# Optimization experiments

Measured on AMD Instinct MI355X. Metric: run time of the kernel, lower is better.

The kernel has to match this reference:

```python
import jax, jax.numpy as jnp
import numpy as np
from jax import lax

THRESH = 1.0
MIN_VMEM = -1.0

def _conv(x, w, stride):
    # x: [N,C,H,W], w: [O,I,kh,kw]
    return lax.conv_general_dilated(
        x, w, window_strides=(stride, stride), padding=((1, 1), (1, 1)),
        dimension_numbers=("NCHW", "OIHW", "NCHW"))

def _avgpool2(x):
    n, c, h, w = x.shape
    return x.reshape(n, c, h // 2, 2, w // 2, 2).mean(axis=(3, 5))

def _iaf(x_bt, B, T):
    # x_bt: [B*T, ...] -> sinabs IAFSqueeze: reshape to [B,T,...], scan over T.
    feat = x_bt.shape[1:]
    seq = x_bt.reshape((B, T) + feat)
    seq_t = jnp.moveaxis(seq, 1, 0)  # [T, B, ...]

    def step(v, u):
        v = v + u                              # integrate
        s = (v >= THRESH).astype(v.dtype)      # SingleSpike
        v = v * (1.0 - s)                      # MembraneReset -> 0
        v = jnp.maximum(v, MIN_VMEM)           # min_v_mem clamp
        return v, s

    v0 = jnp.zeros(seq_t.shape[1:], dtype=x_bt.dtype)
    _, spikes = lax.scan(step, v0, seq_t)      # spikes: [T, B, ...]
    return jnp.moveaxis(spikes, 0, 1).reshape((B * T,) + feat)

def setup_inputs() -> dict:
    key = jax.random.key(0)
    k0, k1, k2, k3, k4 = jax.random.split(key, 5)
    x = jax.random.normal(k0, (25, 40, 2, 128, 128), jnp.float32)
    w1 = jax.random.normal(k1, (8, 2, 3, 3), jnp.float32) * 0.3
    w2 = jax.random.normal(k2, (16, 8, 3, 3), jnp.float32) * 0.2
    w3 = jax.random.normal(k3, (64, 1024), jnp.float32) * 0.1
    w4 = jax.random.normal(k4, (11, 64), jnp.float32) * 0.2
    return {"x": x, "w1": w1, "w2": w2, "w3": w3, "w4": w4}

def reference(x, w1, w2, w3, w4):
    B, T, C, H, W = x.shape
    h = x.reshape(B * T, C, H, W)
    h = _conv(h, w1, 2)          # [BT, 8, 64, 64]
    h = _iaf(h, B, T)
    h = _avgpool2(h)             # [BT, 8, 32, 32]
    h = _conv(h, w2, 2)          # [BT, 16, 16, 16]
    h = _iaf(h, B, T)
    h = _avgpool2(h)             # [BT, 16, 8, 8]
    h = h.reshape(B * T, -1)     # [BT, 1024]
    h = h @ w3.T                 # [BT, 64]
    h = _iaf(h, B, T)
    h = h @ w4.T                 # [BT, 11]
    h = _iaf(h, B, T)
    return h.reshape(B, T, -1)
```

## Files before the change

### kernel.cpp

```cpp
#include <hip/hip_runtime.h>

#define THRESH 1.0f
#define MIN_VMEM -1.0f

__device__ __forceinline__ float iaf_step(float& v, float u) {
    v += u;
    float s = (v >= THRESH) ? 1.f : 0.f;
    v = (s > 0.f) ? 0.f : v;
    v = fmaxf(v, MIN_VMEM);
    return s;
}

__global__ __launch_bounds__(64) void k1_conv1_iaf_pool(
        const float* __restrict__ x, const float* __restrict__ w1,
        float* __restrict__ ws1) {
    const int lane = threadIdx.x;
    const int S = blockIdx.x;
    const int chunk = S >> 5;
    const int r = S & 31;
    const int g = r >> 3;
    const int u = chunk * 8 + (r & 7);
    const int b = u >> 5;
    const int q = u & 31;
    const bool q0 = (q == 0);

    float w[2][18];
    #pragma unroll
    for (int j = 0; j < 2; j++)
        #pragma unroll
        for (int k = 0; k < 18; k++)
            w[j][k] = w1[(2 * g + j) * 18 + k];

    const int iy0 = 4 * q - 1;
    int roff[10];
    #pragma unroll
    for (int r2 = 0; r2 < 10; r2++) {
        const int ci = r2 / 5, rr = r2 % 5;
        roff[r2] = ci * 16384 + max(iy0 + rr, 0) * 128;
    }
    const float* xfl = x + (size_t)(b * 40) * 32768 + lane * 2;

    float vA[2], vB[2];
    #pragma unroll
    for (int j = 0; j < 2; j++) { vA[j] = 0.f; vB[j] = 0.f; }

    #pragma unroll 2
    for (int t = 0; t < 40; t++) {
        const float* xt = xfl + (size_t)t * 32768;
        float2 F[10];
        #pragma unroll
        for (int m = 0; m < 10; m++)
            F[m] = *(const float2*)(xt + roff[m]);
        if (q0) { F[0] = make_float2(0.f, 0.f); F[5] = make_float2(0.f, 0.f); }
        float xm[10];
        #pragma unroll
        for (int r2 = 0; r2 < 10; r2++) {
            const float up = __shfl_up(F[r2].y, 1);
            xm[r2] = (lane == 0) ? 0.f : up;
        }
        float preA[2], preB[2];
        #pragma unroll
        for (int j = 0; j < 2; j++) { preA[j] = 0.f; preB[j] = 0.f; }
        #pragma unroll
        for (int ci = 0; ci < 2; ci++)
            #pragma unroll
            for (int ky = 0; ky < 3; ky++) {
                const int rA = ci * 5 + ky;
                const int rB = rA + 2;
                #pragma unroll
                for (int j = 0; j < 2; j++) {
                    const float w0 = w[j][ci * 9 + ky * 3 + 0];
                    const float w1v = w[j][ci * 9 + ky * 3 + 1];
                    const float w2v = w[j][ci * 9 + ky * 3 + 2];
                    preA[j] += xm[rA] * w0 + F[rA].x * w1v + F[rA].y * w2v;
                    preB[j] += xm[rB] * w0 + F[rB].x * w1v + F[rB].y * w2v;
                }
            }
        const size_t nbase = ((size_t)(b * 40 + t) * 8 + 2 * g) * 1024 + q * 32;
        #pragma unroll
        for (int j = 0; j < 2; j++) {
            float s = iaf_step(vA[j], preA[j]) + iaf_step(vB[j], preB[j]);
            s += __shfl_down(s, 1);
            if (!(lane & 1))
                ws1[nbase + (size_t)j * 1024 + (lane >> 1)] = s * 0.25f;
        }
    }
}

#define K2_CIS 1224

__global__ __launch_bounds__(256) void k2a_conv2(
        const float* __restrict__ ws1, const float* __restrict__ w2,
        float* __restrict__ u2) {
    __shared__ float F[8 * K2_CIS];
    const int n = blockIdx.x;
    const int tid = threadIdx.x;

    for (int i = tid; i < 8 * K2_CIS; i += 256) F[i] = 0.f;
    __syncthreads();
    const float4* src = (const float4*)(ws1 + (size_t)n * 8192);
    #pragma unroll
    for (int k = 0; k < 8; k++) {
        const int i = tid + 256 * k;
        const float4 q = src[i];
        const int ci = i >> 8;
        const int rr = i & 255;
        const int r = rr >> 3, c4 = rr & 7;
        float* d = &F[ci * K2_CIS + (r + 1) * 36 + 1 + 4 * c4];
        d[0] = q.x; d[1] = q.y; d[2] = q.z; d[3] = q.w;
    }
    __syncthreads();

    const int wv = tid >> 6;
    const int ln = tid & 63;
    const int oy = ln >> 2;
    const int ox4 = ln & 3;

    float acc[4][4];
    #pragma unroll
    for (int j = 0; j < 4; j++)
        #pragma unroll
        for (int k = 0; k < 4; k++) acc[j][k] = 0.f;

    #pragma unroll
    for (int ci = 0; ci < 8; ci++) {
        float q[3][9];
        const int base = ci * K2_CIS + (2 * oy) * 36 + 8 * ox4;
        #pragma unroll
        for (int ky = 0; ky < 3; ky++) {
            const float4 qa = *(const float4*)&F[base + ky * 36];
            const float4 qb = *(const float4*)&F[base + ky * 36 + 4];
            q[ky][0] = qa.x; q[ky][1] = qa.y; q[ky][2] = qa.z; q[ky][3] = qa.w;
            q[ky][4] = qb.x; q[ky][5] = qb.y; q[ky][6] = qb.z; q[ky][7] = qb.w;
            q[ky][8] = F[base + ky * 36 + 8];
        }
        #pragma unroll
        for (int j = 0; j < 4; j++) {
            const int co_u = __builtin_amdgcn_readfirstlane(4 * wv + j);
            const float* wb = w2 + co_u * 72 + ci * 9;
            float wm[9];
            #pragma unroll
            for (int m = 0; m < 9; m++) wm[m] = wb[m];
            #pragma unroll
            for (int k = 0; k < 4; k++)
                #pragma unroll
                for (int ky = 0; ky < 3; ky++)
                    #pragma unroll
                    for (int kx = 0; kx < 3; kx++)
                        acc[j][k] += q[ky][2 * k + kx] * wm[ky * 3 + kx];
        }
    }
    float* db = u2 + (size_t)n * 4096 + oy * 16 + 4 * ox4;
    #pragma unroll
    for (int j = 0; j < 4; j++) {
        const int co = 4 * wv + j;
        *(float4*)(db + co * 256) =
            make_float4(acc[j][0], acc[j][1], acc[j][2], acc[j][3]);
    }
}

__global__ __launch_bounds__(64) void k2b_scan(
        const float* __restrict__ u2, float* __restrict__ ws2) {
    const int id = blockIdx.x * 64 + threadIdx.x;
    const int b = id >> 10;
    const int c = (id >> 6) & 15;
    const int pp = id & 63;
    const int py = pp >> 3, px = pp & 7;
    const float* base = u2 + (size_t)(b * 40) * 4096 + c * 256
                      + (2 * py) * 16 + 2 * px;
    float* ob = ws2 + (size_t)(b * 40) * 1024 + c * 64 + py * 8 + px;

    float v0 = 0.f, v1 = 0.f, v2 = 0.f, v3 = 0.f;
    float2 P[2][8][2];
    #pragma unroll
    for (int tt = 0; tt < 8; tt++) {
        const float* nb = base + (size_t)tt * 4096;
        P[0][tt][0] = *(const float2*)(nb);
        P[0][tt][1] = *(const float2*)(nb + 16);
    }
    #pragma unroll
    for (int bt = 0; bt < 5; bt++) {
        if (bt < 4) {
            #pragma unroll
            for (int tt = 0; tt < 8; tt++) {
                const float* nb = base + (size_t)(8 * (bt + 1) + tt) * 4096;
                P[(bt + 1) & 1][tt][0] = *(const float2*)(nb);
                P[(bt + 1) & 1][tt][1] = *(const float2*)(nb + 16);
            }
        }
        #pragma unroll
        for (int tt = 0; tt < 8; tt++) {
            const float2 b0 = P[bt & 1][tt][0];
            const float2 b1 = P[bt & 1][tt][1];
            const float s = iaf_step(v0, b0.x) + iaf_step(v1, b0.y)
                          + iaf_step(v2, b1.x) + iaf_step(v3, b1.y);
            ob[(size_t)(8 * bt + tt) * 1024] = s * 0.25f;
        }
    }
}

__global__ __launch_bounds__(256) void k3_fc1(
        const float* __restrict__ ws2, const float* __restrict__ w3,
        float* __restrict__ ws3) {
    __shared__ float rows[2048];
    const int n0 = blockIdx.x * 2;
    const int tid = threadIdx.x;
    const float4* s = (const float4*)(ws2 + (size_t)n0 * 1024);
    #pragma unroll
    for (int k = 0; k < 2; k++)
        ((float4*)rows)[tid + 256 * k] = s[tid + 256 * k];
    __syncthreads();
    const int o = tid >> 2, ko = tid & 3;
    const float4* wp = (const float4*)(w3 + (size_t)o * 1024 + ko * 256);
    const float4* r0 = (const float4*)(rows + ko * 256);
    const float4* r1 = (const float4*)(rows + 1024 + ko * 256);
    float a0 = 0.f, a1 = 0.f;
    #pragma unroll 8
    for (int j = 0; j < 64; j++) {
        const float4 wv = wp[j];
        const float4 q0 = r0[j], q1 = r1[j];
        a0 += q0.x * wv.x + q0.y * wv.y + q0.z * wv.z + q0.w * wv.w;
        a1 += q1.x * wv.x + q1.y * wv.y + q1.z * wv.z + q1.w * wv.w;
    }
    a0 += __shfl_xor(a0, 1); a0 += __shfl_xor(a0, 2);
    a1 += __shfl_xor(a1, 1); a1 += __shfl_xor(a1, 2);
    if (ko == 0) {
        ws3[(size_t)(n0 + 0) * 64 + o] = a0;
        ws3[(size_t)(n0 + 1) * 64 + o] = a1;
    }
}

__global__ __launch_bounds__(256) void k4_iaf_fc2_iaf(
        const float* __restrict__ ws3, const float* __restrict__ w4,
        float* __restrict__ out) {
    __shared__ float sld[2560];
    __shared__ float pre[40 * 12];
    __shared__ float w4s[704];
    const int b = blockIdx.x, tid = threadIdx.x;

    const float4* src = (const float4*)(ws3 + (size_t)b * 2560);
    for (int i = tid; i < 640; i += 256) ((float4*)sld)[i] = src[i];
    for (int i = tid; i < 176; i += 256) ((float4*)w4s)[i] = ((const float4*)w4)[i];
    __syncthreads();
    if (tid < 64) {
        float v1 = 0.f;
        #pragma unroll
        for (int t = 0; t < 40; t++)
            sld[t * 64 + tid] = iaf_step(v1, sld[t * 64 + tid]);
    }
    __syncthreads();
    for (int idx = tid; idx < 440; idx += 256) {
        const int t = idx % 40, o = idx / 40;
        const float4* spr = (const float4*)(sld + t * 64);
        const float4* wr = (const float4*)(w4s + o * 64);
        float acc = 0.f;
        #pragma unroll
        for (int qq = 0; qq < 16; qq++) {
            const float4 a = spr[qq], ww = wr[qq];
            acc += a.x * ww.x + a.y * ww.y + a.z * ww.z + a.w * ww.w;
        }
        pre[t * 12 + o] = acc;
    }
    __syncthreads();
    if (tid < 11) {
        float v2 = 0.f;
        for (int t = 0; t < 40; t++)
            out[(size_t)(b * 40 + t) * 11 + tid] = iaf_step(v2, pre[t * 12 + tid]);
    }
}

extern "C" void kernel_launch(void* const* d_in, const int* in_sizes, int n_in,
                              void* d_out, int out_size, void* d_ws, size_t ws_size,
                              hipStream_t stream) {
    const float* x  = (const float*)d_in[0];
    const float* w1 = (const float*)d_in[1];
    const float* w2 = (const float*)d_in[2];
    const float* w3 = (const float*)d_in[3];
    const float* w4 = (const float*)d_in[4];
    float* out = (float*)d_out;

    float* ws1 = (float*)d_ws;
    float* ws2 = ws1 + 8192000;
    float* ws3 = ws2 + 1024000;
    float* u2;
    if (ws_size >= (size_t)(8192000 + 1024000 + 64000 + 4096000) * 4)
        u2 = ws3 + 64000;
    else
        u2 = (float*)d_in[0];

    k1_conv1_iaf_pool<<<3200, 64, 0, stream>>>(x, w1, ws1);
    k2a_conv2<<<1000, 256, 0, stream>>>(ws1, w2, u2);
    k2b_scan<<<400, 64, 0, stream>>>(u2, ws2);
    k3_fc1<<<500, 256, 0, stream>>>(ws2, w3, ws3);
    k4_iaf_fc2_iaf<<<25, 256, 0, stream>>>(ws3, w4, out);
}
```

Baseline: 271.9 us.

## Software-pipeline conv1 input loads and widen the second IAF scan kernel

The first kernel now double-buffers input rows across timesteps, issuing loads for step t+2 while computing step t+1, so global load latency overlaps with the serial IAF recurrence. The second scan kernel switches from 64 threads each handling a 2x2 pool window to 256 threads each scanning a single pixel. The pooling sum is done with wave shuffles, which gives four times the thread-level parallelism and coalesced scalar loads. In exchange, the last iterations issue redundant clamped loads, and the scan kernel now performs extra shuffles and three quarters of its lanes do no stores.

```diff
diff --git a/kernel.cpp b/kernel.cpp
--- a/kernel.cpp
+++ b/kernel.cpp
@@ -9,6 +9,44 @@
     v = (s > 0.f) ? 0.f : v;
     v = fmaxf(v, MIN_VMEM);
     return s;
+}
+
+__device__ __forceinline__ void k1_compute(
+        float2 (&F)[10], const bool q0, const int lane,
+        const float (&w)[2][18], float (&vA)[2], float (&vB)[2],
+        float* __restrict__ ws1, const size_t nbase) {
+    if (q0) { F[0] = make_float2(0.f, 0.f); F[5] = make_float2(0.f, 0.f); }
+    float xm[10];
+    #pragma unroll
+    for (int r = 0; r < 10; r++) {
+        const float up = __shfl_up(F[r].y, 1);
+        xm[r] = (lane == 0) ? 0.f : up;
+    }
+    float preA[2], preB[2];
+    #pragma unroll
+    for (int j = 0; j < 2; j++) { preA[j] = 0.f; preB[j] = 0.f; }
+    #pragma unroll
+    for (int ci = 0; ci < 2; ci++)
+        #pragma unroll
+        for (int ky = 0; ky < 3; ky++) {
+            const int rA = ci * 5 + ky;
+            const int rB = rA + 2;
+            #pragma unroll
+            for (int j = 0; j < 2; j++) {
+                const float w0 = w[j][ci * 9 + ky * 3 + 0];
+                const float w1v = w[j][ci * 9 + ky * 3 + 1];
+                const float w2v = w[j][ci * 9 + ky * 3 + 2];
+                preA[j] += xm[rA] * w0 + F[rA].x * w1v + F[rA].y * w2v;
+                preB[j] += xm[rB] * w0 + F[rB].x * w1v + F[rB].y * w2v;
+            }
+        }
+    #pragma unroll
+    for (int j = 0; j < 2; j++) {
+        float s = iaf_step(vA[j], preA[j]) + iaf_step(vB[j], preB[j]);
+        s += __shfl_down(s, 1);
+        if (!(lane & 1))
+            ws1[nbase + (size_t)j * 1024 + (lane >> 1)] = s * 0.25f;
+    }
 }
 
 __global__ __launch_bounds__(64) void k1_conv1_iaf_pool(
@@ -44,45 +82,32 @@
     #pragma unroll
     for (int j = 0; j < 2; j++) { vA[j] = 0.f; vB[j] = 0.f; }
 
-    #pragma unroll 2
-    for (int t = 0; t < 40; t++) {
-        const float* xt = xfl + (size_t)t * 32768;
-        float2 F[10];
-        #pragma unroll
-        for (int m = 0; m < 10; m++)
-            F[m] = *(const float2*)(xt + roff[m]);
-        if (q0) { F[0] = make_float2(0.f, 0.f); F[5] = make_float2(0.f, 0.f); }
-        float xm[10];
-        #pragma unroll
-        for (int r2 = 0; r2 < 10; r2++) {
-            const float up = __shfl_up(F[r2].y, 1);
-            xm[r2] = (lane == 0) ? 0.f : up;
-        }
-        float preA[2], preB[2];
-        #pragma unroll
-        for (int j = 0; j < 2; j++) { preA[j] = 0.f; preB[j] = 0.f; }
-        #pragma unroll
-        for (int ci = 0; ci < 2; ci++)
-            #pragma unroll
-            for (int ky = 0; ky < 3; ky++) {
-                const int rA = ci * 5 + ky;
-                const int rB = rA + 2;
-                #pragma unroll
-                for (int j = 0; j < 2; j++) {
-                    const float w0 = w[j][ci * 9 + ky * 3 + 0];
-                    const float w1v = w[j][ci * 9 + ky * 3 + 1];
-                    const float w2v = w[j][ci * 9 + ky * 3 + 2];
-                    preA[j] += xm[rA] * w0 + F[rA].x * w1v + F[rA].y * w2v;
-                    preB[j] += xm[rB] * w0 + F[rB].x * w1v + F[rB].y * w2v;
-                }
-            }
-        const size_t nbase = ((size_t)(b * 40 + t) * 8 + 2 * g) * 1024 + q * 32;
-        #pragma unroll
-        for (int j = 0; j < 2; j++) {
-            float s = iaf_step(vA[j], preA[j]) + iaf_step(vB[j], preB[j]);
-            s += __shfl_down(s, 1);
-            if (!(lane & 1))
-                ws1[nbase + (size_t)j * 1024 + (lane >> 1)] = s * 0.25f;
+    const size_t obase = ((size_t)(b * 40) * 8 + 2 * g) * 1024 + q * 32;
+
+    float2 FA[10], FB[10];
+    #pragma unroll
+    for (int m = 0; m < 10; m++)
+        FA[m] = *(const float2*)(xfl + roff[m]);
+    #pragma unroll
+    for (int m = 0; m < 10; m++)
+        FB[m] = *(const float2*)(xfl + (size_t)32768 + roff[m]);
+
+    for (int tt = 0; tt < 20; tt++) {
+        const int t0 = 2 * tt;
+        k1_compute(FA, q0, lane, w, vA, vB, ws1, obase + (size_t)t0 * 8192);
+        {
+            const float* xn = xfl + (size_t)min(t0 + 2, 39) * 32768;
+            #pragma unroll
+            for (int m = 0; m < 10; m++)
+                FA[m] = *(const float2*)(xn + roff[m]);
+        }
+        k1_compute(FB, q0, lane, w, vA, vB, ws1,
+                   obase + (size_t)(t0 + 1) * 8192);
+        {
+            const float* xn = xfl + (size_t)min(t0 + 3, 39) * 32768;
+            #pragma unroll
+            for (int m = 0; m < 10; m++)
+                FB[m] = *(const float2*)(xn + roff[m]);
         }
     }
 }
@@ -159,42 +184,37 @@
     }
 }
 
-__global__ __launch_bounds__(64) void k2b_scan(
+__global__ __launch_bounds__(256) void k2b_scan(
         const float* __restrict__ u2, float* __restrict__ ws2) {
-    const int id = blockIdx.x * 64 + threadIdx.x;
-    const int b = id >> 10;
-    const int c = (id >> 6) & 15;
-    const int pp = id & 63;
-    const int py = pp >> 3, px = pp & 7;
-    const float* base = u2 + (size_t)(b * 40) * 4096 + c * 256
-                      + (2 * py) * 16 + 2 * px;
-    float* ob = ws2 + (size_t)(b * 40) * 1024 + c * 64 + py * 8 + px;
-
-    float v0 = 0.f, v1 = 0.f, v2 = 0.f, v3 = 0.f;
-    float2 P[2][8][2];
-    #pragma unroll
-    for (int tt = 0; tt < 8; tt++) {
-        const float* nb = base + (size_t)tt * 4096;
-        P[0][tt][0] = *(const float2*)(nb);
-        P[0][tt][1] = *(const float2*)(nb + 16);
-    }
+    const int blk = blockIdx.x;
+    const int b = blk >> 4;
+    const int c = blk & 15;
+    const int tid = threadIdx.x;
+    const int ty = tid >> 4, tx = tid & 15;
+    const bool red = ((ty & 1) == 0) && ((tx & 1) == 0);
+    const int po = (ty >> 1) * 8 + (tx >> 1);
+    const float* base = u2 + (size_t)(b * 40) * 4096 + c * 256 + tid;
+    float* ob = ws2 + (size_t)(b * 40) * 1024 + c * 64 + po;
+
+    float v = 0.f;
+    float P[2][8];
+    #pragma unroll
+    for (int tt = 0; tt < 8; tt++)
+        P[0][tt] = base[(size_t)tt * 4096];
     #pragma unroll
     for (int bt = 0; bt < 5; bt++) {
         if (bt < 4) {
             #pragma unroll
-            for (int tt = 0; tt < 8; tt++) {
-                const float* nb = base + (size_t)(8 * (bt + 1) + tt) * 4096;
-                P[(bt + 1) & 1][tt][0] = *(const float2*)(nb);
-                P[(bt + 1) & 1][tt][1] = *(const float2*)(nb + 16);
-            }
+            for (int tt = 0; tt < 8; tt++)
+                P[(bt + 1) & 1][tt] = base[(size_t)(8 * (bt + 1) + tt) * 4096];
         }
         #pragma unroll
         for (int tt = 0; tt < 8; tt++) {
-            const float2 b0 = P[bt & 1][tt][0];
-            const float2 b1 = P[bt & 1][tt][1];
-            const float s = iaf_step(v0, b0.x) + iaf_step(v1, b0.y)
-                          + iaf_step(v2, b1.x) + iaf_step(v3, b1.y);
-            ob[(size_t)(8 * bt + tt) * 1024] = s * 0.25f;
+            const float s = iaf_step(v, P[bt & 1][tt]);
+            float r = s + __shfl_down(s, 1);
+            r += __shfl_down(r, 16);
+            if (red)
+                ob[(size_t)(8 * bt + tt) * 1024] = r * 0.25f;
         }
     }
 }
@@ -290,7 +310,7 @@
 
     k1_conv1_iaf_pool<<<3200, 64, 0, stream>>>(x, w1, ws1);
     k2a_conv2<<<1000, 256, 0, stream>>>(ws1, w2, u2);
-    k2b_scan<<<400, 64, 0, stream>>>(u2, ws2);
+    k2b_scan<<<400, 256, 0, stream>>>(u2, ws2);
     k3_fc1<<<500, 256, 0, stream>>>(ws2, w3, ws3);
     k4_iaf_fc2_iaf<<<25, 256, 0, stream>>>(ws3, w4, out);
 }
```

After: 270.8 us. No clear change (-0.4%).
